# Kernel tuning notes

Hardware: AMD Instinct MI355X
Metric: run time of the kernel (lower is better)

The kernel has to match this reference:

```python
import jax, jax.numpy as jnp
import numpy as np

E = 1024      # h_dim
H = 16        # num_heads
D = E // H    # head_dim = 64
O = 1024      # o_dim == q_dim
EPS = 1e-5


def _rotate_half(x):
    d = x.shape[-1]
    x1, x2 = x[..., : d // 2], x[..., d // 2 :]
    return jnp.concatenate([-x2, x1], axis=-1)


def setup_inputs() -> dict:
    key = jax.random.key(0)
    ks = jax.random.split(key, 12)
    B, S = 8, 1024
    s = 0.02
    return {
        "query": jax.random.normal(ks[0], (B, S, O), jnp.float32),
        "key": jax.random.normal(ks[1], (B, S, O), jnp.float32),
        "value": jax.random.normal(ks[2], (B, S, O), jnp.float32),
        "Wq": jax.random.normal(ks[3], (E, O), jnp.float32) * s,
        "Wk": jax.random.normal(ks[4], (E, O), jnp.float32) * s,
        "Wv": jax.random.normal(ks[5], (E, O), jnp.float32) * s,
        "in_proj_w": jax.random.normal(ks[6], (3 * E, E), jnp.float32) * s,
        "out_proj_w": jax.random.normal(ks[7], (E, E), jnp.float32) * s,
        "proj_w": jax.random.normal(ks[8], (O, E), jnp.float32) * s,
        "gamma": jnp.ones((O,), jnp.float32),
        "beta": jnp.zeros((O,), jnp.float32),
    }


def reference(query, key, value, Wq, Wk, Wv, in_proj_w, out_proj_w, proj_w, gamma, beta):
    B, S, _ = query.shape
    # [B,S,*] -> [S,B,*] then bias-free linears
    q = jnp.swapaxes(query, 0, 1) @ Wq.T  # [S,B,E]
    k = jnp.swapaxes(key, 0, 1) @ Wk.T
    v = jnp.swapaxes(value, 0, 1) @ Wv.T

    # RoPE (faithful quirk: positions indexed along the BATCH axis B)
    inv_freq = 1.0 / (10000.0 ** (jnp.arange(0, D, 2, dtype=jnp.float32) / D))
    t = jnp.arange(B, dtype=jnp.float32)
    freqs = t[:, None] * inv_freq[None, :]            # [B, D/2]
    emb = jnp.concatenate([freqs, freqs], axis=-1)    # [B, D]
    cos = jnp.cos(emb)[None, :, None, :]              # [1,B,1,D]
    sin = jnp.sin(emb)[None, :, None, :]

    q4 = q.reshape(S, B, H, D)
    k4 = k.reshape(S, B, H, D)
    q_emb = (q4 * cos + _rotate_half(q4) * sin).reshape(S, B, E)
    k_emb = (k4 * cos + _rotate_half(k4) * sin).reshape(S, B, E)

    # nn.MultiheadAttention (bias=False, batch_first=False)
    Wqa, Wka, Wva = in_proj_w[:E], in_proj_w[E : 2 * E], in_proj_w[2 * E :]
    qp = (q_emb @ Wqa.T).reshape(S, B, H, D)
    kp = (k_emb @ Wka.T).reshape(S, B, H, D)
    vp = (v @ Wva.T).reshape(S, B, H, D)

    scale = 1.0 / np.sqrt(D).astype(np.float32)
    scores = jnp.einsum("sbhd,tbhd->bhst", qp, kp) * scale  # [B,H,S,S]
    attn = jax.nn.softmax(scores, axis=-1)
    o = jnp.einsum("bhst,tbhd->sbhd", attn, vp).reshape(S, B, E)
    o = o @ out_proj_w.T                                     # [S,B,E]

    # output proj + residual + LayerNorm
    ob = jnp.swapaxes(o, 0, 1) @ proj_w.T                    # [B,S,O]
    x = query + ob
    mu = jnp.mean(x, axis=-1, keepdims=True)
    var = jnp.mean((x - mu) ** 2, axis=-1, keepdims=True)
    return (x - mu) * jax.lax.rsqrt(var + EPS) * gamma + beta
```

## Files before the change

kernel.cpp:

```cpp
#include <hip/hip_runtime.h>
#include <hip/hip_bf16.h>
#include <stdint.h>

typedef __bf16 bf16;
typedef __attribute__((ext_vector_type(8))) __bf16 bf16x8;
typedef __attribute__((ext_vector_type(4))) float f32x4;

#define NEG_LN10K_32 (-0.28782313662425575f)

__device__ __forceinline__ bf16x8 cvt8(f32x4 a, f32x4 b) {
    bf16x8 r;
    r[0] = (bf16)a[0]; r[1] = (bf16)a[1]; r[2] = (bf16)a[2]; r[3] = (bf16)a[3];
    r[4] = (bf16)b[0]; r[5] = (bf16)b[1]; r[6] = (bf16)b[2]; r[7] = (bf16)b[3];
    return r;
}

__device__ __forceinline__ void async_copy16(bf16* lds, const bf16* g) {
    __builtin_amdgcn_global_load_lds((const __attribute__((address_space(1))) void*)g,
                                     (__attribute__((address_space(3))) void*)lds, 16, 0, 0);
}

__global__ __launch_bounds__(256) void wconv6(
    const float* __restrict__ s0, const float* __restrict__ s1, const float* __restrict__ s2,
    const float* __restrict__ s3, const float* __restrict__ s4, const float* __restrict__ s5,
    bf16* __restrict__ d0, bf16* __restrict__ d1, bf16* __restrict__ d2,
    bf16* __restrict__ d3, bf16* __restrict__ d4, bf16* __restrict__ d5)
{
    const int z = blockIdx.z;
    const float* src; bf16* dst;
    switch (z) {
        case 0: src = s0; dst = d0; break;
        case 1: src = s1; dst = d1; break;
        case 2: src = s2; dst = d2; break;
        case 3: src = s3; dst = d3; break;
        case 4: src = s4; dst = d4; break;
        default: src = s5; dst = d5; break;
    }
    const size_t i = ((size_t)blockIdx.x * 256 + threadIdx.x) * 8;
    *(bf16x8*)(dst + i) = cvt8(*(const f32x4*)(src + i), *(const f32x4*)(src + i + 4));
}

__global__ __launch_bounds__(256) void prepT(
    const float* __restrict__ in0, const float* __restrict__ in1,
    bf16* __restrict__ out0, bf16* __restrict__ out1)
{
    const float* in = blockIdx.z ? in1 : in0;
    bf16* out       = blockIdx.z ? out1 : out0;
    __shared__ float tile[64 * 65];
    const int t  = threadIdx.x;
    const int i0 = blockIdx.y * 64, j0 = blockIdx.x * 64;
    const int r  = t >> 2, cg = (t & 3) * 16;
#pragma unroll
    for (int c = 0; c < 16; c += 4) {
        const f32x4 v = *(const f32x4*)(in + (size_t)(i0 + r) * 1024 + j0 + cg + c);
        tile[r * 65 + cg + c + 0] = v[0];
        tile[r * 65 + cg + c + 1] = v[1];
        tile[r * 65 + cg + c + 2] = v[2];
        tile[r * 65 + cg + c + 3] = v[3];
    }
    __syncthreads();
    bf16x8 o0v, o1v;
#pragma unroll
    for (int ii = 0; ii < 8; ++ii) {
        o0v[ii] = (bf16)tile[(cg + ii) * 65 + r];
        o1v[ii] = (bf16)tile[(cg + 8 + ii) * 65 + r];
    }
    bf16* dst = out + (size_t)(j0 + r) * 1024 + i0 + cg;
    *(bf16x8*)dst       = o0v;
    *(bf16x8*)(dst + 8) = o1v;
}

template<int AF32, int WF32>
__global__ __launch_bounds__(256) void gemm_bt(
    const void* __restrict__ A0v, const void* __restrict__ A1v, const void* __restrict__ A2v,
    const void* __restrict__ W0v, const void* __restrict__ W1v, const void* __restrict__ W2v,
    bf16* __restrict__ C0, bf16* __restrict__ C1, bf16* __restrict__ C2,
    const float* __restrict__ R0, int rope_mask)
{
    const int z = blockIdx.z;
    const void* Av = (z == 0) ? A0v : ((z == 1) ? A1v : A2v);
    const void* Wp = (z == 0) ? W0v : ((z == 1) ? W1v : W2v);
    bf16*       C  = (z == 0) ? C0 : ((z == 1) ? C1 : C2);
    const float* R = (z == 0) ? R0 : nullptr;
    const bool doRope = ((rope_mask >> z) & 1) != 0;

    __shared__ __attribute__((aligned(16))) bf16 sA[128 * 32];
    __shared__ __attribute__((aligned(16))) bf16 sB[128 * 32];

    const int t    = threadIdx.x;
    const int w    = t >> 6;
    const int lane = t & 63;
    const int l16  = lane & 15;
    const int quad = lane >> 4;
    const int wrow = w >> 1;
    const int wcol = w & 1;

    int m0, n0;
    if (gridDim.y == 64) {
        const int fs   = blockIdx.y * 8 + blockIdx.x;
        const int xcd  = fs & 7;
        const int slot = fs >> 3;
        m0 = ((xcd << 3) | (slot >> 3)) * 128;
        n0 = (slot & 7) * 128;
    } else {
        m0 = blockIdx.y * 128;
        n0 = blockIdx.x * 128;
    }

    const size_t aOff = (size_t)(m0 + (t >> 2)) * 1024 + (t & 3) * 8;
    const size_t wOff = (size_t)(n0 + (t >> 2)) * 1024 + (t & 3) * 8;

    f32x4 acc[4][4];
#pragma unroll
    for (int i = 0; i < 4; ++i)
#pragma unroll
        for (int j = 0; j < 4; ++j)
            acc[i][j] = (f32x4){0.f, 0.f, 0.f, 0.f};

    for (int k0 = 0; k0 < 1024; k0 += 32) {
        bf16x8 va0, va1, vb0, vb1;
        if (AF32) {
            const float* g = (const float*)Av;
            va0 = cvt8(*(const f32x4*)(g + aOff + k0),             *(const f32x4*)(g + aOff + k0 + 4));
            va1 = cvt8(*(const f32x4*)(g + aOff + 64 * 1024 + k0), *(const f32x4*)(g + aOff + 64 * 1024 + k0 + 4));
        }
        if (WF32) {
            const float* g = (const float*)Wp;
            vb0 = cvt8(*(const f32x4*)(g + wOff + k0),             *(const f32x4*)(g + wOff + k0 + 4));
            vb1 = cvt8(*(const f32x4*)(g + wOff + 64 * 1024 + k0), *(const f32x4*)(g + wOff + 64 * 1024 + k0 + 4));
        }
        __syncthreads();
        if (AF32) {
            *(bf16x8*)&sA[t * 8]        = va0;
            *(bf16x8*)&sA[t * 8 + 2048] = va1;
        } else {
            const bf16* g = (const bf16*)Av;
            async_copy16(sA + w * 512,        g + aOff + k0);
            async_copy16(sA + w * 512 + 2048, g + aOff + 64 * 1024 + k0);
        }
        if (WF32) {
            *(bf16x8*)&sB[t * 8]        = vb0;
            *(bf16x8*)&sB[t * 8 + 2048] = vb1;
        } else {
            const bf16* g = (const bf16*)Wp;
            async_copy16(sB + w * 512,        g + wOff + k0);
            async_copy16(sB + w * 512 + 2048, g + wOff + 64 * 1024 + k0);
        }
        __syncthreads();

        bf16x8 af[4], bw[4];
#pragma unroll
        for (int mi = 0; mi < 4; ++mi)
            af[mi] = *(const bf16x8*)&sA[(wrow * 64 + mi * 16 + l16) * 32 + quad * 8];
#pragma unroll
        for (int ni = 0; ni < 4; ++ni)
            bw[ni] = *(const bf16x8*)&sB[(wcol * 64 + ni * 16 + l16) * 32 + quad * 8];
#pragma unroll
        for (int mi = 0; mi < 4; ++mi)
#pragma unroll
            for (int ni = 0; ni < 4; ++ni)
                acc[mi][ni] = __builtin_amdgcn_mfma_f32_16x16x32_bf16(af[mi], bw[ni], acc[mi][ni], 0, 0, 0);
    }

    if (doRope) {
        const float bb = (float)(m0 >> 10);
        float s0, c0v, s1, c1v;
        sincosf(bb * expf((float)l16 * NEG_LN10K_32), &s0, &c0v);
        sincosf(bb * expf((float)(16 + l16) * NEG_LN10K_32), &s1, &c1v);
#pragma unroll
        for (int mi = 0; mi < 4; ++mi) {
#pragma unroll
            for (int r = 0; r < 4; ++r) {
                float x1 = acc[mi][0][r], x2 = acc[mi][2][r];
                acc[mi][0][r] = x1 * c0v - x2 * s0;
                acc[mi][2][r] = x2 * c0v + x1 * s0;
                x1 = acc[mi][1][r]; x2 = acc[mi][3][r];
                acc[mi][1][r] = x1 * c1v - x2 * s1;
                acc[mi][3][r] = x2 * c1v + x1 * s1;
            }
        }
    }

#pragma unroll
    for (int mi = 0; mi < 4; ++mi) {
#pragma unroll
        for (int ni = 0; ni < 4; ++ni) {
            const int col = n0 + wcol * 64 + ni * 16 + l16;
#pragma unroll
            for (int r = 0; r < 4; ++r) {
                const int row = m0 + wrow * 64 + mi * 16 + quad * 4 + r;
                float v = acc[mi][ni][r];
                if (R) v += R[(size_t)row * 1024 + col];
                C[(size_t)row * 1024 + col] = (bf16)v;
            }
        }
    }
}

__global__ __launch_bounds__(256) void attn_kernel(
    bf16* __restrict__ QP, const bf16* __restrict__ KP, const bf16* __restrict__ VP)
{
    const int fs   = blockIdx.y * 8 + blockIdx.x;
    const int xcd  = fs & 7;
    const int slot = fs >> 3;
    const int qt   = slot & 7;
    const int bh   = (xcd << 4) | (slot >> 3);
    const int tb = (bh >> 4) << 10;
    const int fb = (bh & 15) << 6;

    __shared__ __attribute__((aligned(16))) bf16 sK0[64 * 32];
    __shared__ __attribute__((aligned(16))) bf16 sK1[64 * 32];
    __shared__ __attribute__((aligned(16))) bf16 sVt[64 * 72];
    __shared__ __attribute__((aligned(16))) bf16 sP[4][32 * 72];

    const int t    = threadIdx.x;
    const int w    = t >> 6;
    const int lane = t & 63;
    const int l16  = lane & 15;
    const int quad = lane >> 4;

    bf16x8 qf[2][2];
#pragma unroll
    for (int mi = 0; mi < 2; ++mi)
#pragma unroll
        for (int kd = 0; kd < 2; ++kd)
            qf[mi][kd] = *(const bf16x8*)&QP[(size_t)(tb + qt * 128 + w * 32 + mi * 16 + l16) * 1024
                                            + fb + kd * 32 + quad * 8];

    f32x4 oacc[2][4];
#pragma unroll
    for (int i = 0; i < 2; ++i)
#pragma unroll
        for (int j = 0; j < 4; ++j)
            oacc[i][j] = (f32x4){0.f, 0.f, 0.f, 0.f};
    float psum[2][4];
#pragma unroll
    for (int i = 0; i < 2; ++i)
#pragma unroll
        for (int r = 0; r < 4; ++r) psum[i][r] = 0.f;

    for (int kt = 0; kt < 16; ++kt) {
        const bf16* kRow = KP + (size_t)(tb + kt * 64 + (t >> 2)) * 1024 + fb + (t & 3) * 8;
        const bf16x8 vk0 = *(const bf16x8*)(kRow);
        const bf16x8 vk1 = *(const bf16x8*)(kRow + 32);
        const bf16* vRow = VP + (size_t)(tb + kt * 64 + lane) * 1024 + fb;
        const bf16x8 vv0 = *(const bf16x8*)(vRow + w * 8);
        const bf16x8 vv1 = *(const bf16x8*)(vRow + (w + 4) * 8);

        __syncthreads();
        *(bf16x8*)&sK0[t * 8] = vk0;
        *(bf16x8*)&sK1[t * 8] = vk1;
#pragma unroll
        for (int j = 0; j < 8; ++j) sVt[(w * 8 + j) * 72 + lane]       = vv0[j];
#pragma unroll
        for (int j = 0; j < 8; ++j) sVt[((w + 4) * 8 + j) * 72 + lane] = vv1[j];
        __syncthreads();

        bf16x8 kf[4][2];
#pragma unroll
        for (int ni = 0; ni < 4; ++ni) {
            kf[ni][0] = *(const bf16x8*)&sK0[(ni * 16 + l16) * 32 + quad * 8];
            kf[ni][1] = *(const bf16x8*)&sK1[(ni * 16 + l16) * 32 + quad * 8];
        }
        f32x4 sfr[2][4];
#pragma unroll
        for (int mi = 0; mi < 2; ++mi)
#pragma unroll
            for (int ni = 0; ni < 4; ++ni) {
                f32x4 a = (f32x4){0.f, 0.f, 0.f, 0.f};
                a = __builtin_amdgcn_mfma_f32_16x16x32_bf16(qf[mi][0], kf[ni][0], a, 0, 0, 0);
                a = __builtin_amdgcn_mfma_f32_16x16x32_bf16(qf[mi][1], kf[ni][1], a, 0, 0, 0);
                sfr[mi][ni] = a * 0.125f;
            }

#pragma unroll
        for (int mi = 0; mi < 2; ++mi)
#pragma unroll
            for (int ni = 0; ni < 4; ++ni)
#pragma unroll
                for (int r = 0; r < 4; ++r) {
                    const float p = __expf(sfr[mi][ni][r]);
                    sfr[mi][ni][r] = p;
                    psum[mi][r] += p;
                }

        bf16* sPw = &sP[w][0];
#pragma unroll
        for (int mi = 0; mi < 2; ++mi)
#pragma unroll
            for (int ni = 0; ni < 4; ++ni)
#pragma unroll
                for (int r = 0; r < 4; ++r)
                    sPw[(mi * 16 + quad * 4 + r) * 72 + ni * 16 + l16] = (bf16)sfr[mi][ni][r];
        asm volatile("s_waitcnt lgkmcnt(0)" ::: "memory");

#pragma unroll
        for (int kd = 0; kd < 2; ++kd) {
            bf16x8 pf[2], vf[4];
#pragma unroll
            for (int mi = 0; mi < 2; ++mi)
                pf[mi] = *(const bf16x8*)&sPw[(mi * 16 + l16) * 72 + kd * 32 + quad * 8];
#pragma unroll
            for (int di = 0; di < 4; ++di)
                vf[di] = *(const bf16x8*)&sVt[(di * 16 + l16) * 72 + kd * 32 + quad * 8];
#pragma unroll
            for (int mi = 0; mi < 2; ++mi)
#pragma unroll
                for (int di = 0; di < 4; ++di)
                    oacc[mi][di] = __builtin_amdgcn_mfma_f32_16x16x32_bf16(pf[mi], vf[di], oacc[mi][di], 0, 0, 0);
        }
    }

#pragma unroll
    for (int mi = 0; mi < 2; ++mi) {
#pragma unroll
        for (int r = 0; r < 4; ++r) {
            float l = psum[mi][r];
            l += __shfl_xor(l, 1);
            l += __shfl_xor(l, 2);
            l += __shfl_xor(l, 4);
            l += __shfl_xor(l, 8);
            const float inv = 1.f / l;
            const int row = tb + qt * 128 + w * 32 + mi * 16 + quad * 4 + r;
#pragma unroll
            for (int di = 0; di < 4; ++di) {
                const int col = fb + di * 16 + l16;
                QP[(size_t)row * 1024 + col] = (bf16)(oacc[mi][di][r] * inv);
            }
        }
    }
}

__global__ __launch_bounds__(128) void ln_kernel(const bf16* __restrict__ X,
                                                 const float* __restrict__ G,
                                                 const float* __restrict__ Bt,
                                                 float* __restrict__ Y)
{
    const int row = blockIdx.x;
    const int t   = threadIdx.x;
    const size_t base = (size_t)row * 1024 + t * 8;
    const bf16x8 xv = *(const bf16x8*)(X + base);
    float f[8];
    float s = 0.f, s2 = 0.f;
#pragma unroll
    for (int j = 0; j < 8; ++j) { f[j] = (float)xv[j]; s += f[j]; s2 += f[j] * f[j]; }
#pragma unroll
    for (int off = 1; off < 64; off <<= 1) { s += __shfl_xor(s, off); s2 += __shfl_xor(s2, off); }
    __shared__ float ss[2], ssq[2];
    if ((t & 63) == 0) { ss[t >> 6] = s; ssq[t >> 6] = s2; }
    __syncthreads();
    s  = ss[0] + ss[1];
    s2 = ssq[0] + ssq[1];
    const float mu  = s * (1.f / 1024.f);
    const float inv = rsqrtf(s2 * (1.f / 1024.f) - mu * mu + 1e-5f);
    const f32x4 g0 = *(const f32x4*)(G + t * 8);
    const f32x4 g1 = *(const f32x4*)(G + t * 8 + 4);
    const f32x4 b0 = *(const f32x4*)(Bt + t * 8);
    const f32x4 b1 = *(const f32x4*)(Bt + t * 8 + 4);
    f32x4 y0, y1;
#pragma unroll
    for (int j = 0; j < 4; ++j) {
        y0[j] = (f[j]     - mu) * inv * g0[j] + b0[j];
        y1[j] = (f[j + 4] - mu) * inv * g1[j] + b1[j];
    }
    *(f32x4*)(Y + base)     = y0;
    *(f32x4*)(Y + base + 4) = y1;
}

extern "C" void kernel_launch(void* const* d_in, const int* in_sizes, int n_in,
                              void* d_out, int out_size, void* d_ws, size_t ws_size,
                              hipStream_t stream)
{
    const float* query = (const float*)d_in[0];
    const float* key   = (const float*)d_in[1];
    const float* value = (const float*)d_in[2];
    const float* Wq    = (const float*)d_in[3];
    const float* Wk    = (const float*)d_in[4];
    const float* Wv    = (const float*)d_in[5];
    const float* ipw   = (const float*)d_in[6];
    const float* opw   = (const float*)d_in[7];
    const float* pw    = (const float*)d_in[8];
    const float* gamma = (const float*)d_in[9];
    const float* beta  = (const float*)d_in[10];

    const size_t ACT = (size_t)8192 * 1024;
    const size_t MW  = 1048576;
    bf16* o0 = (bf16*)d_out;
    bf16* o1 = o0 + ACT;

    dim3 blk(256);
    dim3 g3(8, 64, 3);
    dim3 g1(8, 64, 1);
    dim3 ga(8, 128);

    const bool full = ws_size >= (6 * MW + 2 * ACT) * sizeof(bf16);

    if (full) {
        bf16* wq  = (bf16*)d_ws;
        bf16* wk  = wq + MW;
        bf16* wqa = wq + 2 * MW;
        bf16* wka = wq + 3 * MW;
        bf16* Fv  = wq + 4 * MW;
        bf16* Fo  = wq + 5 * MW;
        bf16* sltA = wq + 6 * MW;
        bf16* sltB = sltA + ACT;
        bf16* tWva = sltA;
        bf16* tpw  = sltA + MW;
        bf16* WvT  = sltB;
        bf16* opwT = sltB + MW;

        wconv6<<<dim3(512, 1, 6), blk, 0, stream>>>(
            Wq, Wk, ipw, ipw + MW, ipw + 2 * MW, pw,
            wq, wk, wqa, wka, tWva, tpw);
        prepT<<<dim3(16, 16, 2), blk, 0, stream>>>(Wv, opw, WvT, opwT);
        gemm_bt<0, 0><<<dim3(8, 8, 2), blk, 0, stream>>>(
            tWva, tpw, tpw, WvT, opwT, opwT, Fv, Fo, Fo, nullptr, 0);
        gemm_bt<1, 0><<<g3, blk, 0, stream>>>(query, key, value, wq, wk, Fv,
                                              sltA, sltB, o0, nullptr, 0b011);
        gemm_bt<0, 0><<<g1, blk, 0, stream>>>(sltA, sltA, sltA, wqa, wqa, wqa,
                                              o1, o1, o1, nullptr, 0);
        gemm_bt<0, 0><<<g1, blk, 0, stream>>>(sltB, sltB, sltB, wka, wka, wka,
                                              sltA, sltA, sltA, nullptr, 0);
        attn_kernel<<<ga, blk, 0, stream>>>(o1, sltA, o0);
        gemm_bt<0, 0><<<g1, blk, 0, stream>>>(o1, o1, o1, Fo, Fo, Fo,
                                              sltB, sltB, sltB, query, 0);
        ln_kernel<<<8192, 128, 0, stream>>>(sltB, gamma, beta, (float*)d_out);
    } else {
        bf16* b0 = (bf16*)d_ws;
        bf16* b1 = b0 + ACT;
        gemm_bt<1, 1><<<g3, blk, 0, stream>>>(query, key, value, Wq, Wk, Wv,
                                              b0, b1, o0, nullptr, 0b011);
        gemm_bt<0, 1><<<g1, blk, 0, stream>>>(o0, o0, o0, ipw + 2 * MW, ipw, ipw,
                                              o1, o1, o1, nullptr, 0);
        gemm_bt<0, 1><<<g1, blk, 0, stream>>>(b0, b0, b0, ipw, ipw, ipw,
                                              o0, o0, o0, nullptr, 0);
        gemm_bt<0, 1><<<g1, blk, 0, stream>>>(b1, b1, b1, ipw + MW, ipw, ipw,
                                              b0, b0, b0, nullptr, 0);
        attn_kernel<<<ga, blk, 0, stream>>>(o0, b0, o1);
        gemm_bt<0, 1><<<g1, blk, 0, stream>>>(o0, o0, o0, opw, opw, opw,
                                              b0, b0, b0, nullptr, 0);
        gemm_bt<0, 1><<<g1, blk, 0, stream>>>(b0, b0, b0, pw, pw, pw,
                                              b1, b1, b1, query, 0);
        ln_kernel<<<8192, 128, 0, stream>>>(b1, gamma, beta, (float*)d_out);
    }
}
```

Before: 455.4 us.

## Add 256x128-tile 512-thread GEMM with triple-buffered async staging for projections

Introduces a new GEMM kernel with 256x128 output tiles, 8 waves per block, and a three-stage LDS ring fed by direct global-to-LDS loads (double-buffered register staging for fp32 A). It replaces the 128x128 GEMM in the main projection, in-projection and output-projection launches on the full-workspace path. The larger tile is meant to improve operand reuse and keep more loads in flight to hide memory latency. In exchange it uses more LDS per block, which lowers occupancy, and halves the grid, which could leave some compute units underused.

Measured after the change: 467.6 us. 2.7% more time.

```diff
diff --git a/kernel.cpp b/kernel.cpp
--- a/kernel.cpp
+++ b/kernel.cpp
@@ -197,6 +197,178 @@
     }
 }
 
+template<int AF32>
+__global__ __launch_bounds__(512) void gemm256(
+    const void* __restrict__ A0v, const void* __restrict__ A1v, const void* __restrict__ A2v,
+    const bf16* __restrict__ W0, const bf16* __restrict__ W1, const bf16* __restrict__ W2,
+    bf16* __restrict__ C0, bf16* __restrict__ C1, bf16* __restrict__ C2,
+    const float* __restrict__ R0, int rope_mask)
+{
+    const int z = blockIdx.z;
+    const void* Av = (z == 0) ? A0v : ((z == 1) ? A1v : A2v);
+    const bf16* Wp = (z == 0) ? W0 : ((z == 1) ? W1 : W2);
+    bf16*       C  = (z == 0) ? C0 : ((z == 1) ? C1 : C2);
+    const float* R = (z == 0) ? R0 : nullptr;
+    const bool doRope = ((rope_mask >> z) & 1) != 0;
+
+    __shared__ __attribute__((aligned(16))) bf16 sA[(AF32 ? 2 : 3) * 16384];
+    __shared__ __attribute__((aligned(16))) bf16 sB[3 * 8192];
+
+    const int t    = threadIdx.x;
+    const int w    = t >> 6;
+    const int lane = t & 63;
+    const int l16  = lane & 15;
+    const int quad = lane >> 4;
+    const int wr   = w >> 1;
+    const int wc   = w & 1;
+
+    const int fs = blockIdx.y * 8 + blockIdx.x;
+    const int m0 = ((fs & 7) * 4 + ((fs >> 3) >> 3)) * 256;
+    const int n0 = ((fs >> 3) & 7) * 128;
+
+    size_t offA[4];
+#pragma unroll
+    for (int s = 0; s < 4; ++s) {
+        const int gi  = (w * 4 + s) * 64 + lane;
+        const int row = gi >> 3;
+        const int xc  = (gi & 7) ^ (row & 7);
+        offA[s] = (size_t)(m0 + row) * 1024 + xc * 8;
+    }
+    size_t offB[2];
+#pragma unroll
+    for (int s = 0; s < 2; ++s) {
+        const int gi  = (w * 2 + s) * 64 + lane;
+        const int row = gi >> 3;
+        const int xc  = (gi & 7) ^ (row & 7);
+        offB[s] = (size_t)(n0 + row) * 1024 + xc * 8;
+    }
+
+    auto stageB = [&](int kt, int buf) {
+#pragma unroll
+        for (int s = 0; s < 2; ++s)
+            async_copy16(sB + buf * 8192 + (w * 2 + s) * 512, Wp + offB[s] + kt * 64);
+    };
+    auto stageA16 = [&](int kt, int buf) {
+        const bf16* gA = (const bf16*)Av;
+#pragma unroll
+        for (int s = 0; s < 4; ++s)
+            async_copy16(sA + buf * 16384 + (w * 4 + s) * 512, gA + offA[s] + kt * 64);
+    };
+
+    f32x4 ra0[4][2], ra1[4][2];
+    auto loadA32 = [&](int kt, f32x4 (&rr)[4][2]) {
+        const float* gA = (const float*)Av;
+#pragma unroll
+        for (int s = 0; s < 4; ++s) {
+            rr[s][0] = *(const f32x4*)(gA + offA[s] + kt * 64);
+            rr[s][1] = *(const f32x4*)(gA + offA[s] + kt * 64 + 4);
+        }
+    };
+    auto writeA32 = [&](int buf, f32x4 (&rr)[4][2]) {
+#pragma unroll
+        for (int s = 0; s < 4; ++s)
+            *(bf16x8*)(sA + buf * 16384 + (w * 4 + s) * 512 + lane * 8) = cvt8(rr[s][0], rr[s][1]);
+    };
+
+    f32x4 acc[4][4];
+#pragma unroll
+    for (int i = 0; i < 4; ++i)
+#pragma unroll
+        for (int j = 0; j < 4; ++j)
+            acc[i][j] = (f32x4){0.f, 0.f, 0.f, 0.f};
+
+    if (AF32) {
+        loadA32(0, ra0); stageB(0, 0);
+        loadA32(1, ra1); stageB(1, 1);
+        writeA32(0, ra0);
+    } else {
+        stageA16(0, 0); stageB(0, 0);
+        stageA16(1, 1); stageB(1, 1);
+    }
+
+    for (int tk = 0; tk < 16; ++tk) {
+        if (AF32) {
+            if (tk + 1 < 16) {
+                if (tk & 1) writeA32(0, ra0); else writeA32(1, ra1);
+            }
+            if (tk + 2 < 16) {
+                if (tk & 1) loadA32(tk + 2, ra1); else loadA32(tk + 2, ra0);
+                stageB(tk + 2, (tk + 2) % 3);
+            }
+            if (tk == 15) asm volatile("s_waitcnt vmcnt(0) lgkmcnt(0)\ns_barrier" ::: "memory");
+            else          asm volatile("s_waitcnt lgkmcnt(0)\ns_barrier" ::: "memory");
+        } else {
+            if (tk + 2 < 16) {
+                stageA16(tk + 2, (tk + 2) % 3);
+                stageB(tk + 2, (tk + 2) % 3);
+            }
+            if (tk < 14)       asm volatile("s_waitcnt vmcnt(12) lgkmcnt(0)\ns_barrier" ::: "memory");
+            else if (tk == 14) asm volatile("s_waitcnt vmcnt(6) lgkmcnt(0)\ns_barrier" ::: "memory");
+            else               asm volatile("s_waitcnt vmcnt(0) lgkmcnt(0)\ns_barrier" ::: "memory");
+        }
+
+        const bf16* bufA = sA + (AF32 ? (tk & 1) : (tk % 3)) * 16384;
+        const bf16* bufB = sB + (tk % 3) * 8192;
+
+#pragma unroll
+        for (int kk = 0; kk < 2; ++kk) {
+            bf16x8 af[4], bw[4];
+#pragma unroll
+            for (int mi = 0; mi < 4; ++mi) {
+                const int r_ = wr * 64 + mi * 16 + l16;
+                af[mi] = *(const bf16x8*)&bufA[r_ * 64 + (((kk * 4 + quad) ^ (l16 & 7)) * 8)];
+            }
+#pragma unroll
+            for (int ni = 0; ni < 4; ++ni) {
+                const int r_ = wc * 64 + ni * 16 + l16;
+                bw[ni] = *(const bf16x8*)&bufB[r_ * 64 + (((kk * 4 + quad) ^ (l16 & 7)) * 8)];
+            }
+            __builtin_amdgcn_s_setprio(1);
+#pragma unroll
+            for (int mi = 0; mi < 4; ++mi)
+#pragma unroll
+                for (int ni = 0; ni < 4; ++ni)
+                    acc[mi][ni] = __builtin_amdgcn_mfma_f32_16x16x32_bf16(af[mi], bw[ni], acc[mi][ni], 0, 0, 0);
+            __builtin_amdgcn_s_setprio(0);
+        }
+        asm volatile("s_waitcnt lgkmcnt(0)\ns_barrier" ::: "memory");
+    }
+
+    if (doRope) {
+        const float bb = (float)(m0 >> 10);
+        float s0, c0v, s1, c1v;
+        sincosf(bb * expf((float)l16 * NEG_LN10K_32), &s0, &c0v);
+        sincosf(bb * expf((float)(16 + l16) * NEG_LN10K_32), &s1, &c1v);
+#pragma unroll
+        for (int mi = 0; mi < 4; ++mi) {
+#pragma unroll
+            for (int r = 0; r < 4; ++r) {
+                float x1 = acc[mi][0][r], x2 = acc[mi][2][r];
+                acc[mi][0][r] = x1 * c0v - x2 * s0;
+                acc[mi][2][r] = x2 * c0v + x1 * s0;
+                x1 = acc[mi][1][r]; x2 = acc[mi][3][r];
+                acc[mi][1][r] = x1 * c1v - x2 * s1;
+                acc[mi][3][r] = x2 * c1v + x1 * s1;
+            }
+        }
+    }
+
+#pragma unroll
+    for (int mi = 0; mi < 4; ++mi) {
+#pragma unroll
+        for (int ni = 0; ni < 4; ++ni) {
+            const int col = n0 + wc * 64 + ni * 16 + l16;
+#pragma unroll
+            for (int r = 0; r < 4; ++r) {
+                const int row = m0 + wr * 64 + mi * 16 + quad * 4 + r;
+                float v = acc[mi][ni][r];
+                if (R) v += R[(size_t)row * 1024 + col];
+                C[(size_t)row * 1024 + col] = (bf16)v;
+            }
+        }
+    }
+}
+
 __global__ __launch_bounds__(256) void attn_kernel(
     bf16* __restrict__ QP, const bf16* __restrict__ KP, const bf16* __restrict__ VP)
 {
@@ -389,9 +561,12 @@
     bf16* o1 = o0 + ACT;
 
     dim3 blk(256);
+    dim3 blk512(512);
     dim3 g3(8, 64, 3);
     dim3 g1(8, 64, 1);
     dim3 ga(8, 128);
+    dim3 q3(8, 32, 3);
+    dim3 q1(8, 32, 1);
 
     const bool full = ws_size >= (6 * MW + 2 * ACT) * sizeof(bf16);
 
@@ -415,14 +590,14 @@
         prepT<<<dim3(16, 16, 2), blk, 0, stream>>>(Wv, opw, WvT, opwT);
         gemm_bt<0, 0><<<dim3(8, 8, 2), blk, 0, stream>>>(
             tWva, tpw, tpw, WvT, opwT, opwT, Fv, Fo, Fo, nullptr, 0);
-        gemm_bt<1, 0><<<g3, blk, 0, stream>>>(query, key, value, wq, wk, Fv,
+        gemm256<1><<<q3, blk512, 0, stream>>>(query, key, value, wq, wk, Fv,
                                               sltA, sltB, o0, nullptr, 0b011);
-        gemm_bt<0, 0><<<g1, blk, 0, stream>>>(sltA, sltA, sltA, wqa, wqa, wqa,
+        gemm256<0><<<q1, blk512, 0, stream>>>(sltA, sltA, sltA, wqa, wqa, wqa,
                                               o1, o1, o1, nullptr, 0);
-        gemm_bt<0, 0><<<g1, blk, 0, stream>>>(sltB, sltB, sltB, wka, wka, wka,
+        gemm256<0><<<q1, blk512, 0, stream>>>(sltB, sltB, sltB, wka, wka, wka,
                                               sltA, sltA, sltA, nullptr, 0);
         attn_kernel<<<ga, blk, 0, stream>>>(o1, sltA, o0);
-        gemm_bt<0, 0><<<g1, blk, 0, stream>>>(o1, o1, o1, Fo, Fo, Fo,
+        gemm256<0><<<q1, blk512, 0, stream>>>(o1, o1, o1, Fo, Fo, Fo,
                                               sltB, sltB, sltB, query, 0);
         ln_kernel<<<8192, 128, 0, stream>>>(sltB, gamma, beta, (float*)d_out);
     } else {
```
